# Optimization experiments

Measured on AMD Instinct MI355X. Metric: run time of the kernel, lower is better.

## Reference

```python
import jax, jax.numpy as jnp
import numpy as np
from jax import lax

B, N, K, M, NC = 64, 1024, 20, 256, 40  # clouds, points/cloud, knn k, fps points (ratio 0.25), classes
EPS = 1e-5


def setup_inputs() -> dict:
    key = jax.random.key(0)
    ks = jax.random.split(key, 6)
    w = lambda k, s: jax.random.normal(k, s, jnp.float32) * 0.05
    return {
        "pos": jax.random.normal(ks[0], (B * N, 3), jnp.float32),
        "w1": w(ks[1], (64, 3)), "b1": jnp.zeros(64, jnp.float32),
        "g1": jnp.ones(64, jnp.float32), "be1": jnp.zeros(64, jnp.float32),
        "w2": w(ks[2], (64, 64)), "b2": jnp.zeros(64, jnp.float32),
        "g2": jnp.ones(64, jnp.float32), "be2": jnp.zeros(64, jnp.float32),
        "w_nn1": w(ks[3], (512, 64)), "b_nn1": jnp.zeros(512, jnp.float32),
        "g_bn2": jnp.ones(512, jnp.float32), "be_bn2": jnp.zeros(512, jnp.float32),
        "w_nn4": w(ks[4], (NC, 512)), "b_nn4": jnp.zeros(NC, jnp.float32),
    }


def _knn_idx(p):  # p: [N,3] -> [N,K] neighbor indices, self excluded (loop=False)
    d = jnp.sum(p * p, -1)[:, None] + jnp.sum(p * p, -1)[None, :] - 2.0 * (p @ p.T)
    d = d.at[jnp.arange(N), jnp.arange(N)].set(jnp.inf)
    _, idx = lax.top_k(-d, K)
    return idx


def _fps_idx(p):  # p: [N,3] -> [M] farthest-point-sampling indices (deterministic start at 0)
    def step(carry, _):
        dist, last = carry
        d = jnp.sum((p - p[last]) ** 2, -1)
        dist = jnp.minimum(dist, d)
        nxt = jnp.argmax(dist).astype(jnp.int32)
        return (dist, nxt), nxt
    init = (jnp.full((N,), 1e38, jnp.float32), jnp.int32(0))
    _, idxs = lax.scan(step, init, None, length=M - 1)
    return jnp.concatenate([jnp.zeros((1,), jnp.int32), idxs])


def _bn(x, g, b, axes):  # batch-norm with batch statistics (training mode)
    m = jnp.mean(x, axes, keepdims=True)
    v = jnp.var(x, axes, keepdims=True)
    return (x - m) * lax.rsqrt(v + EPS) * g + b


def reference(pos, w1, b1, g1, be1, w2, b2, g2, be2,
              w_nn1, b_nn1, g_bn2, be_bn2, w_nn4, b_nn4):
    p = pos.reshape(B, N, 3)
    idx = jax.vmap(_knn_idx)(p)                     # [B,N,K]
    nbr = jax.vmap(lambda pb, ib: pb[ib])(p, idx)   # [B,N,K,3]
    rel = nbr - p[:, :, None, :]                    # edge features (relative positions)
    h = jax.nn.relu(jnp.einsum('bnkc,fc->bnkf', rel, w1) + b1)
    h = _bn(h, g1, be1, (0, 1, 2))
    h = jax.nn.relu(jnp.einsum('bnkf,gf->bnkg', h, w2) + b2)
    h = _bn(h, g2, be2, (0, 1, 2))
    feat = jnp.max(h, axis=2)                       # [B,N,64] edge-conv max aggregation
    fidx = jax.vmap(_fps_idx)(p)                    # [B,M]
    f = jnp.take_along_axis(feat, fidx[:, :, None], axis=1)  # [B,M,64]
    y = jnp.einsum('bmf,hf->bmh', f, w_nn1) + b_nn1  # [B,M,512]
    y = jnp.max(y, axis=1)                           # [B,512]
    y = jax.nn.relu(y)
    y = _bn(y, g_bn2, be_bn2, (0,))
    y = y @ w_nn4.T + b_nn4                          # [B,40]
    return jax.nn.log_softmax(y, axis=1)
```

## Files before the change

kernel.cpp:

```cpp
#include <hip/hip_runtime.h>
#include <hip/hip_bf16.h>
#include <cfloat>
#include <math.h>

#define BB 64
#define NN 1024
#define KNN 20
#define MM 256
#define CC 64
#define HH 512
#define NCLS 40
#define EPSF 1e-5f
#define CNT1 (BB*NN*KNN)

#define IDX_OFF    0
#define MAXH2_OFF  (IDX_OFF + BB*NN*KNN)
#define FIDX_OFF   (MAXH2_OFF + BB*NN*CC)
#define Y_OFF      (FIDX_OFF + BB*MM)
#define ACC_OFF    (Y_OFF + BB*HH)
#define W2T_OFF    (ACC_OFF + 256)
#define B2F_OFF    (W2T_OFF + CC*CC)
#define S2_OFF     (B2F_OFF + CC)
#define T2_OFF     (S2_OFF + CC)
#define S3_OFF     (T2_OFF + CC)
#define T3_OFF     (S3_OFF + HH)

typedef __attribute__((ext_vector_type(8)))  short short8;
typedef __attribute__((ext_vector_type(16))) float f32x16;

static __device__ __forceinline__ unsigned short f2bf(float f) {
  unsigned u = __float_as_uint(f);
  unsigned r = (u + 0x7fffu + ((u >> 16) & 1u)) >> 16;
  return (unsigned short)r;
}

__global__ __launch_bounds__(256) void knn_fps_kernel(const float* __restrict__ pos,
                                                      int* __restrict__ idxg,
                                                      int* __restrict__ fidxg) {
  __shared__ float4 pj[NN];
  if (blockIdx.x >= BB) {
    int blk = blockIdx.x - BB;
    int b  = blk >> 5;
    int nb = blk & 31;
    const float* pb = pos + (size_t)b * NN * 3;
    for (int i = threadIdx.x; i < NN; i += 256) {
      float x = pb[i*3+0], y = pb[i*3+1], z = pb[i*3+2];
      pj[i] = make_float4(x, y, z, (x*x + y*y) + z*z);
    }
    __syncthreads();
    int lane = threadIdx.x & 63;
    int wv   = threadIdx.x >> 6;
    unsigned long long lmask_lt = (1ULL << lane) - 1ULL;

    for (int t = 0; t < 8; ++t) {
      int i = nb*32 + wv*8 + t;
      float4 pi = pj[i];
      unsigned u[16];
#pragma unroll
      for (int q = 0; q < 16; ++q) {
        int j = q*64 + lane;
        float4 pw = pj[j];
        float d = pi.w + pw.w - 2.0f*(pi.x*pw.x + pi.y*pw.y + pi.z*pw.z);
        unsigned bits = __float_as_uint(d);
        bits = (bits & 0x80000000u) ? ~bits : (bits | 0x80000000u);
        if (j == i) bits = 0xFFFFFFFFu;
        u[q] = bits;
      }
      unsigned lmin = u[0];
#pragma unroll
      for (int q = 1; q < 16; ++q) lmin = (u[q] < lmin) ? u[q] : lmin;
      unsigned rmin = lmin, rmax = lmin;
#define KNN_DPP_STEP(C) { \
      unsigned t1 = (unsigned)__builtin_amdgcn_update_dpp((int)rmin, (int)rmin, (C), 0xf, 0xf, false); \
      unsigned t2 = (unsigned)__builtin_amdgcn_update_dpp((int)rmax, (int)rmax, (C), 0xf, 0xf, false); \
      rmin = (t1 < rmin) ? t1 : rmin; rmax = (t2 > rmax) ? t2 : rmax; }
      KNN_DPP_STEP(0x111)
      KNN_DPP_STEP(0x112)
      KNN_DPP_STEP(0x114)
      KNN_DPP_STEP(0x118)
      KNN_DPP_STEP(0x142)
      KNN_DPP_STEP(0x143)
#undef KNN_DPP_STEP
      unsigned plo = ((unsigned)__builtin_amdgcn_readlane((int)rmin, 63)) >> 16;
      unsigned phi = ((unsigned)__builtin_amdgcn_readlane((int)rmax, 63)) >> 16;
      int cntHi = -1;
      while (plo < phi) {
        unsigned pmid = (plo + phi) >> 1;
        unsigned tmid = (pmid << 16) | 0xFFFFu;
        int cnt = 0;
#pragma unroll
        for (int q = 0; q < 16; ++q)
          cnt += (int)__popcll(__ballot(u[q] <= tmid));
        if (cnt >= KNN) { phi = pmid; cntHi = cnt; } else plo = pmid + 1;
      }
      unsigned tstar = (phi << 16) | 0xFFFFu;
      unsigned bbase = phi << 16;
      int* op = idxg + (size_t)(b*NN + i) * KNN;
      if (cntHi < 0) {
        cntHi = 0;
#pragma unroll
        for (int q = 0; q < 16; ++q)
          cntHi += (int)__popcll(__ballot(u[q] <= tstar));
      }
      if (cntHi == KNN) {
        int base = 0;
#pragma unroll
        for (int q = 0; q < 16; ++q) {
          bool pred = (u[q] <= tstar);
          unsigned long long mask = __ballot((int)pred);
          if (pred) op[base + (int)__popcll(mask & lmask_lt)] = q*64 + lane;
          base += (int)__popcll(mask);
        }
      } else {
        unsigned lo2 = bbase, hi2 = tstar;
        while (lo2 < hi2) {
          unsigned mid = lo2 + ((hi2 - lo2) >> 1);
          int cnt = 0;
#pragma unroll
          for (int q = 0; q < 16; ++q)
            cnt += (int)__popcll(__ballot(u[q] <= mid));
          if (cnt >= KNN) hi2 = mid; else lo2 = mid + 1;
        }
        unsigned xstar = lo2;
        int base = 0;
#pragma unroll
        for (int q = 0; q < 16; ++q) {
          bool pred = (u[q] < xstar);
          unsigned long long mask = __ballot((int)pred);
          if (pred) op[base + (int)__popcll(mask & lmask_lt)] = q*64 + lane;
          base += (int)__popcll(mask);
        }
        for (int q = 0; q < 16 && base < KNN; ++q) {
          bool pred = (u[q] == xstar);
          unsigned long long mask = __ballot((int)pred);
          if (pred) {
            int pos_ = base + (int)__popcll(mask & lmask_lt);
            if (pos_ < KNN) op[pos_] = q*64 + lane;
          }
          base += (int)__popcll(mask);
        }
      }
    }
  } else {
    int b = blockIdx.x;
    const float* pb = pos + (size_t)b * NN * 3;
    for (int i = threadIdx.x; i < NN; i += 256)
      pj[i] = make_float4(pb[i*3], pb[i*3+1], pb[i*3+2], 0.f);
    __syncthreads();
    if (threadIdx.x >= 64) return;
    int lane = threadIdx.x;
    float px[16], py[16], pz[16], dist[16];
#pragma unroll
    for (int q = 0; q < 16; ++q) {
      float4 p = pj[q*64 + lane];
      px[q] = p.x; py[q] = p.y; pz[q] = p.z;
      dist[q] = 1e38f;
    }
    if (lane == 0) fidxg[b*MM] = 0;
    int cur = 0;
    for (int m = 1; m < MM; ++m) {
      float4 cp = pj[cur];
#pragma unroll
      for (int q = 0; q < 16; ++q) {
        float dx = __fsub_rn(px[q], cp.x);
        float dy = __fsub_rn(py[q], cp.y);
        float dz = __fsub_rn(pz[q], cp.z);
        float dd = __fadd_rn(__fadd_rn(__fmul_rn(dx,dx), __fmul_rn(dy,dy)), __fmul_rn(dz,dz));
        dist[q] = fminf(dist[q], dd);
      }
      float t8[8];
#pragma unroll
      for (int q = 0; q < 8; ++q) t8[q] = fmaxf(dist[q], dist[q + 8]);
#pragma unroll
      for (int q = 0; q < 4; ++q) t8[q] = fmaxf(t8[q], t8[q + 4]);
      float lmax = fmaxf(fmaxf(t8[0], t8[1]), fmaxf(t8[2], t8[3]));
      float r = lmax;
#define FPS_VMAX_STEP(C) { \
      int tt = __builtin_amdgcn_update_dpp(__float_as_int(r), __float_as_int(r), (C), 0xf, 0xf, false); \
      r = fmaxf(r, __int_as_float(tt)); }
      FPS_VMAX_STEP(0x111)
      FPS_VMAX_STEP(0x112)
      FPS_VMAX_STEP(0x114)
      FPS_VMAX_STEP(0x118)
      FPS_VMAX_STEP(0x142)
      FPS_VMAX_STEP(0x143)
#undef FPS_VMAX_STEP
      float wmax = __int_as_float(__builtin_amdgcn_readlane(__float_as_int(r), 63));
      unsigned ci = 0xFFFFFFFFu;
#pragma unroll
      for (int q = 15; q >= 0; --q)
        if (dist[q] == wmax) ci = (unsigned)(q*64 + lane);
#define FPS_IMIN_STEP(C) { \
      unsigned tt = (unsigned)__builtin_amdgcn_update_dpp((int)ci, (int)ci, (C), 0xf, 0xf, false); \
      ci = (tt < ci) ? tt : ci; }
      FPS_IMIN_STEP(0x111)
      FPS_IMIN_STEP(0x112)
      FPS_IMIN_STEP(0x114)
      FPS_IMIN_STEP(0x118)
      FPS_IMIN_STEP(0x142)
      FPS_IMIN_STEP(0x143)
#undef FPS_IMIN_STEP
      cur = (int)(unsigned)__builtin_amdgcn_readlane((int)ci, 63);
      if (lane == 0) fidxg[b*MM + m] = cur;
    }
  }
}

__global__ __launch_bounds__(256) void stats1_kernel(const float* __restrict__ pos,
    const int* __restrict__ idxg, const float* __restrict__ w1,
    const float* __restrict__ b1, float* __restrict__ acc) {
  int b = blockIdx.x >> 4;
  int nb = blockIdx.x & 15;
  __shared__ float px[NN], py[NN], pz[NN];
  __shared__ float relx[4][KNN], rely[4][KNN], relz[4][KNN];
  __shared__ float red[4][CC];
  const float* pb = pos + (size_t)b*NN*3;
  for (int i = threadIdx.x; i < NN; i += 256) {
    px[i] = pb[i*3+0]; py[i] = pb[i*3+1]; pz[i] = pb[i*3+2];
  }
  int c = threadIdx.x & 63, w = threadIdx.x >> 6;
  float w1x = w1[c*3+0], w1y = w1[c*3+1], w1z = w1[c*3+2], b1c = b1[c];
  float s = 0.f, ss = 0.f;
  __syncthreads();
  for (int it = 0; it < 16; ++it) {
    int n0 = nb*64 + it*4;
    if (threadIdx.x < 80) {
      int wv = threadIdx.x / KNN, k = threadIdx.x % KNN;
      int n = n0 + wv;
      int j = idxg[(size_t)(b*NN + n)*KNN + k];
      relx[wv][k] = px[j] - px[n];
      rely[wv][k] = py[j] - py[n];
      relz[wv][k] = pz[j] - pz[n];
    }
    __syncthreads();
#pragma unroll
    for (int k = 0; k < KNN; ++k) {
      float h = fmaxf(relx[w][k]*w1x + rely[w][k]*w1y + relz[w][k]*w1z + b1c, 0.f);
      s += h; ss += h*h;
    }
    __syncthreads();
  }
  red[w][c] = s; __syncthreads();
  if (w == 0) atomicAdd(&acc[c], red[0][c]+red[1][c]+red[2][c]+red[3][c]);
  __syncthreads();
  red[w][c] = ss; __syncthreads();
  if (w == 0) atomicAdd(&acc[64+c], red[0][c]+red[1][c]+red[2][c]+red[3][c]);
}

__global__ void fold1_kernel(const float* __restrict__ acc, const float* __restrict__ g1,
    const float* __restrict__ be1, const float* __restrict__ w2, const float* __restrict__ b2,
    unsigned short* __restrict__ w2bf, float* __restrict__ b2f) {
  __shared__ float s1[CC], t1[CC];
  int tid = threadIdx.x;
  if (tid < CC) {
    float cnt = (float)CNT1;
    float m = acc[tid] / cnt;
    float v = acc[64+tid] / cnt - m*m;
    float sc = g1[tid] * rsqrtf(v + EPSF);
    s1[tid] = sc; t1[tid] = be1[tid] - m*sc;
  }
  __syncthreads();
  int frag = tid >> 6;
  int lane = tid & 63;
  int nt = frag >> 2, ks = frag & 3;
  int cout = nt*32 + (lane & 31);
  int cin0 = ks*16 + (lane >> 5)*8;
  for (int j = 0; j < 8; ++j) {
    int cin = cin0 + j;
    w2bf[((size_t)frag*64 + lane)*8 + j] = f2bf(w2[cout*CC + cin] * s1[cin]);
  }
  if (tid < CC) {
    float accb = b2[tid];
    for (int ci = 0; ci < CC; ++ci) accb += t1[ci]*w2[tid*CC + ci];
    b2f[tid] = accb;
  }
}

__global__ __launch_bounds__(256, 4) void conv2_kernel(const float* __restrict__ pos,
    const int* __restrict__ idxg, const float* __restrict__ w1, const float* __restrict__ b1,
    const unsigned short* __restrict__ w2bf, const float* __restrict__ b2fg,
    float* __restrict__ maxh2, float* __restrict__ acc2) {
  int b = blockIdx.x >> 4;
  int nb = blockIdx.x & 15;
  __shared__ float px[NN], py[NN], pz[NN];
  __shared__ float4 relw[4][KNN];
  __shared__ __align__(16) unsigned short h1s[4][2112];
  __shared__ float redbuf[4][2*CC];
  const float* pb = pos + (size_t)b*NN*3;
  for (int i = threadIdx.x; i < NN; i += 256) {
    px[i] = pb[i*3+0]; py[i] = pb[i*3+1]; pz[i] = pb[i*3+2];
  }
  int lane = threadIdx.x & 63, w = threadIdx.x >> 6;
  int half = lane >> 5, l31 = lane & 31;
  short8 Bf[2][4];
#pragma unroll
  for (int nt = 0; nt < 2; ++nt)
#pragma unroll
    for (int ks = 0; ks < 4; ++ks)
      Bf[nt][ks] = *(const short8*)&w2bf[((size_t)(nt*4+ks)*64 + lane)*8];
  float b2o0 = b2fg[l31], b2o1 = b2fg[32 + l31];
  float w1x = w1[lane*3+0], w1y = w1[lane*3+1], w1z = w1[lane*3+2], b1c = b1[lane];
  unsigned short* hw = h1s[w];
  {
    short8 zz = {0,0,0,0,0,0,0,0};
    for (int z = lane; z < 96; z += 64) {
      int g = z / 12, r = 20 + z % 12;
      *(short8*)&hw[g*264 + r*8] = zz;
    }
  }
  float sA = 0.f, ssA = 0.f, sB = 0.f, ssB = 0.f;
  __syncthreads();
  for (int t = 0; t < 16; ++t) {
    int n = nb*64 + w*16 + t;
    if (lane < KNN) {
      int j = idxg[(size_t)(b*NN + n)*KNN + lane];
      relw[w][lane] = make_float4(px[j]-px[n], py[j]-py[n], pz[j]-pz[n], 0.f);
    }
    int gbase = (lane >> 3)*264 + (lane & 7);
#pragma unroll
    for (int k = 0; k < KNN; ++k) {
      float4 r4 = relw[w][k];
      float h = fmaxf(fmaf(r4.x, w1x, fmaf(r4.y, w1y, fmaf(r4.z, w1z, b1c))), 0.f);
      hw[gbase + k*8] = f2bf(h);
    }
    f32x16 acc0 = {}; f32x16 acc1 = {};
#pragma unroll
    for (int ks = 0; ks < 4; ++ks) {
      short8 A = *(const short8*)&hw[(ks*2 + half)*264 + l31*8];
      acc0 = __builtin_amdgcn_mfma_f32_32x32x16_bf16(A, Bf[0][ks], acc0, 0, 0, 0);
      acc1 = __builtin_amdgcn_mfma_f32_32x32x16_bf16(A, Bf[1][ks], acc1, 0, 0, 0);
    }
    float mx0 = 0.f, mx1 = 0.f;
#pragma unroll
    for (int reg = 0; reg < 8; ++reg) {
      float v0 = fmaxf(acc0[reg] + b2o0, 0.f);
      float v1 = fmaxf(acc1[reg] + b2o1, 0.f);
      sA += v0; ssA += v0*v0; sB += v1; ssB += v1*v1;
      mx0 = fmaxf(mx0, v0); mx1 = fmaxf(mx1, v1);
    }
    if (half == 0) {
#pragma unroll
      for (int reg = 8; reg < 12; ++reg) {
        float v0 = fmaxf(acc0[reg] + b2o0, 0.f);
        float v1 = fmaxf(acc1[reg] + b2o1, 0.f);
        sA += v0; ssA += v0*v0; sB += v1; ssB += v1*v1;
        mx0 = fmaxf(mx0, v0); mx1 = fmaxf(mx1, v1);
      }
    }
    mx0 = fmaxf(mx0, __shfl_xor(mx0, 32, 64));
    mx1 = fmaxf(mx1, __shfl_xor(mx1, 32, 64));
    if (half == 0) {
      float* mp = maxh2 + (size_t)(b*NN + n)*CC;
      mp[l31] = mx0; mp[32 + l31] = mx1;
    }
  }
  sA += __shfl_xor(sA, 32, 64); ssA += __shfl_xor(ssA, 32, 64);
  sB += __shfl_xor(sB, 32, 64); ssB += __shfl_xor(ssB, 32, 64);
  if (half == 0) { redbuf[w][l31] = sA; redbuf[w][32 + l31] = sB; }
  __syncthreads();
  if (w == 0) atomicAdd(&acc2[lane], redbuf[0][lane]+redbuf[1][lane]+redbuf[2][lane]+redbuf[3][lane]);
  __syncthreads();
  if (half == 0) { redbuf[w][l31] = ssA; redbuf[w][32 + l31] = ssB; }
  __syncthreads();
  if (w == 0) atomicAdd(&acc2[64+lane], redbuf[0][lane]+redbuf[1][lane]+redbuf[2][lane]+redbuf[3][lane]);
}

__global__ void fold2_kernel(const float* __restrict__ acc2, const float* __restrict__ g2,
    const float* __restrict__ be2, float* __restrict__ s2, float* __restrict__ t2) {
  int c = threadIdx.x;
  float cnt = (float)CNT1;
  float m = acc2[c]/cnt;
  float v = acc2[64+c]/cnt - m*m;
  float sc = g2[c]*rsqrtf(v+EPSF);
  s2[c] = sc;
  t2[c] = be2[c] - m*sc;
}

__global__ __launch_bounds__(256) void head_kernel(const float* __restrict__ maxh2,
    const int* __restrict__ fidxg, const float* __restrict__ s2g, const float* __restrict__ t2g,
    const float* __restrict__ wnn1, const float* __restrict__ bnn1, float* __restrict__ Y) {
  int b = blockIdx.x >> 2;
  int hc = blockIdx.x & 3;
  __shared__ __align__(16) float ftile[128][CC];
  __shared__ float red2[4][128];
  int hl = threadIdx.x & 63, mseg = threadIdx.x >> 6;
  int hA = hc*128 + hl, hB = hA + 64;
  float4 wva[16], wvb[16];
  const float4* wrA = (const float4*)(wnn1 + (size_t)hA*CC);
  const float4* wrB = (const float4*)(wnn1 + (size_t)hB*CC);
#pragma unroll
  for (int q = 0; q < 16; ++q) { wva[q] = wrA[q]; wvb[q] = wrB[q]; }
  float bestA = -FLT_MAX, bestB = -FLT_MAX;
  const int* fb = fidxg + b*MM;
  for (int chunk = 0; chunk < 2; ++chunk) {
    {
      int row = threadIdx.x & 127, chal = threadIdx.x >> 7;
      int fi = fb[chunk*128 + row];
      const float* src = maxh2 + (size_t)(b*NN + fi)*CC;
      for (int ci = chal*32; ci < chal*32+32; ++ci)
        ftile[row][ci] = s2g[ci]*src[ci] + t2g[ci];
    }
    __syncthreads();
    for (int m = mseg*32; m < mseg*32+32; ++m) {
      float accA = 0.f, accB = 0.f;
#pragma unroll
      for (int cq = 0; cq < 16; ++cq) {
        float4 f = *((const float4*)&ftile[m][cq*4]);
        accA = fmaf(f.x, wva[cq].x, accA);
        accA = fmaf(f.y, wva[cq].y, accA);
        accA = fmaf(f.z, wva[cq].z, accA);
        accA = fmaf(f.w, wva[cq].w, accA);
        accB = fmaf(f.x, wvb[cq].x, accB);
        accB = fmaf(f.y, wvb[cq].y, accB);
        accB = fmaf(f.z, wvb[cq].z, accB);
        accB = fmaf(f.w, wvb[cq].w, accB);
      }
      bestA = fmaxf(bestA, accA);
      bestB = fmaxf(bestB, accB);
    }
    __syncthreads();
  }
  red2[mseg][hl] = bestA;
  red2[mseg][64 + hl] = bestB;
  __syncthreads();
  if (threadIdx.x < 128) {
    int hh = hc*128 + threadIdx.x;
    float v = fmaxf(fmaxf(red2[0][threadIdx.x], red2[1][threadIdx.x]),
                    fmaxf(red2[2][threadIdx.x], red2[3][threadIdx.x])) + bnn1[hh];
    Y[(size_t)b*HH + hh] = fmaxf(v, 0.f);
  }
}

__global__ void bn3_kernel(const float* __restrict__ Y, const float* __restrict__ g,
    const float* __restrict__ be, float* __restrict__ s3, float* __restrict__ t3) {
  int h = blockIdx.x*256 + threadIdx.x;
  float s = 0.f;
  for (int b = 0; b < BB; ++b) s += Y[(size_t)b*HH + h];
  float m = s / (float)BB;
  float v = 0.f;
  for (int b = 0; b < BB; ++b) { float d = Y[(size_t)b*HH + h] - m; v += d*d; }
  v /= (float)BB;
  float sc = g[h] * rsqrtf(v + EPSF);
  s3[h] = sc; t3[h] = be[h] - m*sc;
}

__global__ __launch_bounds__(256) void logits_kernel(const float* __restrict__ Y,
    const float* __restrict__ s3, const float* __restrict__ t3,
    const float* __restrict__ w4, const float* __restrict__ b4, float* __restrict__ out) {
  int b = blockIdx.x;
  __shared__ float ybn[HH];
  __shared__ float lg[NCLS];
  __shared__ float lse;
  for (int hh = threadIdx.x; hh < HH; hh += 256)
    ybn[hh] = Y[(size_t)b*HH + hh]*s3[hh] + t3[hh];
  __syncthreads();
  if (threadIdx.x < NCLS) {
    int j = threadIdx.x;
    float acc = b4[j];
    const float* wr = w4 + (size_t)j*HH;
    for (int ci = 0; ci < HH; ++ci) acc = fmaf(ybn[ci], wr[ci], acc);
    lg[j] = acc;
  }
  __syncthreads();
  if (threadIdx.x == 0) {
    float mx = -FLT_MAX;
    for (int j = 0; j < NCLS; ++j) mx = fmaxf(mx, lg[j]);
    float s = 0.f;
    for (int j = 0; j < NCLS; ++j) s += expf(lg[j] - mx);
    lse = mx + logf(s);
  }
  __syncthreads();
  if (threadIdx.x < NCLS) out[b*NCLS + threadIdx.x] = lg[threadIdx.x] - lse;
}

extern "C" void kernel_launch(void* const* d_in, const int* in_sizes, int n_in,
                              void* d_out, int out_size, void* d_ws, size_t ws_size,
                              hipStream_t stream) {
  const float* pos  = (const float*)d_in[0];
  const float* w1   = (const float*)d_in[1];
  const float* b1   = (const float*)d_in[2];
  const float* g1   = (const float*)d_in[3];
  const float* be1  = (const float*)d_in[4];
  const float* w2   = (const float*)d_in[5];
  const float* b2   = (const float*)d_in[6];
  const float* g2   = (const float*)d_in[7];
  const float* be2  = (const float*)d_in[8];
  const float* wnn1 = (const float*)d_in[9];
  const float* bnn1 = (const float*)d_in[10];
  const float* gbn2 = (const float*)d_in[11];
  const float* bebn2= (const float*)d_in[12];
  const float* wnn4 = (const float*)d_in[13];
  const float* bnn4 = (const float*)d_in[14];
  float* ws = (float*)d_ws;
  int*   idxg  = (int*)(ws + IDX_OFF);
  float* maxh2 = ws + MAXH2_OFF;
  int*   fidxg = (int*)(ws + FIDX_OFF);
  float* Y     = ws + Y_OFF;
  float* acc1  = ws + ACC_OFF;
  float* acc2  = ws + ACC_OFF + 128;
  unsigned short* w2bf = (unsigned short*)(ws + W2T_OFF);
  float* b2f   = ws + B2F_OFF;
  float* s2    = ws + S2_OFF;
  float* t2    = ws + T2_OFF;
  float* s3    = ws + S3_OFF;
  float* t3    = ws + T3_OFF;
  float* outp  = (float*)d_out;

  hipMemsetAsync((void*)(ws + ACC_OFF), 0, 256*sizeof(float), stream);
  knn_fps_kernel<<<BB + BB*32, 256, 0, stream>>>(pos, idxg, fidxg);
  stats1_kernel<<<BB*16, 256, 0, stream>>>(pos, idxg, w1, b1, acc1);
  fold1_kernel<<<1, 512, 0, stream>>>(acc1, g1, be1, w2, b2, w2bf, b2f);
  conv2_kernel<<<BB*16, 256, 0, stream>>>(pos, idxg, w1, b1, w2bf, b2f, maxh2, acc2);
  fold2_kernel<<<1, 64, 0, stream>>>(acc2, g2, be2, s2, t2);
  head_kernel<<<BB*4, 256, 0, stream>>>(maxh2, fidxg, s2, t2, wnn1, bnn1, Y);
  bn3_kernel<<<2, 256, 0, stream>>>(Y, gbn2, bebn2, s3, t3);
  logits_kernel<<<BB, 256, 0, stream>>>(Y, s3, t3, wnn4, bnn4, outp);
}
```

Before: 380.1 us.

## Split serial FPS across three kernels to overlap with KNN and conv stages

The serial farthest-point-sampling loop, which previously ran entirely inside the KNN kernel, is split into three phases (iterations 1-100, 101-150, 151-255). Each phase runs as 64 extra blocks inside the knn, stats1 and conv2 kernels. The running distance array and current index are saved to workspace between phases. The aim is to hide the long single-wave FPS critical path behind the other kernels' work instead of letting it define the knn kernel's tail. The cost is extra state save/restore traffic and extra blocks that compete for CUs in stats1 and conv2.

```diff
diff --git a/kernel.cpp b/kernel.cpp
--- a/kernel.cpp
+++ b/kernel.cpp
@@ -12,6 +12,9 @@
 #define NCLS 40
 #define EPSF 1e-5f
 #define CNT1 (BB*NN*KNN)
+
+#define FPS_R1 101
+#define FPS_R2 151
 
 #define IDX_OFF    0
 #define MAXH2_OFF  (IDX_OFF + BB*NN*KNN)
@@ -24,6 +27,8 @@
 #define T2_OFF     (S2_OFF + CC)
 #define S3_OFF     (T2_OFF + CC)
 #define T3_OFF     (S3_OFF + HH)
+#define FPSD_OFF   (T3_OFF + HH)
+#define FPSC_OFF   (FPSD_OFF + BB*NN)
 
 typedef __attribute__((ext_vector_type(8)))  short short8;
 typedef __attribute__((ext_vector_type(16))) float f32x16;
@@ -34,9 +39,83 @@
   return (unsigned short)r;
 }
 
+static __device__ __forceinline__ void fps_phase(
+    const float* sx, const float* sy, const float* sz,
+    float* fpsd, int* fpsc, int* fidxg, int b, int mStart, int mEnd) {
+  int lane = threadIdx.x;
+  float lx[16], ly[16], lz[16], dist[16];
+#pragma unroll
+  for (int q = 0; q < 16; ++q) {
+    int j = q*64 + lane;
+    lx[q] = sx[j]; ly[q] = sy[j]; lz[q] = sz[j];
+  }
+  int cur;
+  if (mStart <= 1) {
+#pragma unroll
+    for (int q = 0; q < 16; ++q) dist[q] = 1e38f;
+    if (lane == 0) fidxg[b*MM] = 0;
+    cur = 0;
+  } else {
+#pragma unroll
+    for (int q = 0; q < 16; ++q) dist[q] = fpsd[b*NN + q*64 + lane];
+    cur = fpsc[b];
+  }
+  for (int m = mStart; m < mEnd; ++m) {
+    float cpx = sx[cur], cpy = sy[cur], cpz = sz[cur];
+#pragma unroll
+    for (int q = 0; q < 16; ++q) {
+      float dx = __fsub_rn(lx[q], cpx);
+      float dy = __fsub_rn(ly[q], cpy);
+      float dz = __fsub_rn(lz[q], cpz);
+      float dd = __fadd_rn(__fadd_rn(__fmul_rn(dx,dx), __fmul_rn(dy,dy)), __fmul_rn(dz,dz));
+      dist[q] = fminf(dist[q], dd);
+    }
+    float t8[8];
+#pragma unroll
+    for (int q = 0; q < 8; ++q) t8[q] = fmaxf(dist[q], dist[q + 8]);
+#pragma unroll
+    for (int q = 0; q < 4; ++q) t8[q] = fmaxf(t8[q], t8[q + 4]);
+    float r = fmaxf(fmaxf(t8[0], t8[1]), fmaxf(t8[2], t8[3]));
+#define FPS_VMAX_STEP(C) { \
+    int tt = __builtin_amdgcn_update_dpp(__float_as_int(r), __float_as_int(r), (C), 0xf, 0xf, false); \
+    r = fmaxf(r, __int_as_float(tt)); }
+    FPS_VMAX_STEP(0x111)
+    FPS_VMAX_STEP(0x112)
+    FPS_VMAX_STEP(0x114)
+    FPS_VMAX_STEP(0x118)
+    FPS_VMAX_STEP(0x142)
+    FPS_VMAX_STEP(0x143)
+#undef FPS_VMAX_STEP
+    float wmax = __int_as_float(__builtin_amdgcn_readlane(__float_as_int(r), 63));
+    unsigned ci = 0xFFFFFFFFu;
+#pragma unroll
+    for (int q = 15; q >= 0; --q)
+      if (dist[q] == wmax) ci = (unsigned)(q*64 + lane);
+#define FPS_IMIN_STEP(C) { \
+    unsigned tt = (unsigned)__builtin_amdgcn_update_dpp((int)ci, (int)ci, (C), 0xf, 0xf, false); \
+    ci = (tt < ci) ? tt : ci; }
+    FPS_IMIN_STEP(0x111)
+    FPS_IMIN_STEP(0x112)
+    FPS_IMIN_STEP(0x114)
+    FPS_IMIN_STEP(0x118)
+    FPS_IMIN_STEP(0x142)
+    FPS_IMIN_STEP(0x143)
+#undef FPS_IMIN_STEP
+    cur = (int)(unsigned)__builtin_amdgcn_readlane((int)ci, 63);
+    if (lane == 0) fidxg[b*MM + m] = cur;
+  }
+  if (mEnd < MM) {
+#pragma unroll
+    for (int q = 0; q < 16; ++q) fpsd[b*NN + q*64 + lane] = dist[q];
+    if (lane == 0) fpsc[b] = cur;
+  }
+}
+
 __global__ __launch_bounds__(256) void knn_fps_kernel(const float* __restrict__ pos,
                                                       int* __restrict__ idxg,
-                                                      int* __restrict__ fidxg) {
+                                                      int* __restrict__ fidxg,
+                                                      float* __restrict__ fpsd,
+                                                      int* __restrict__ fpsc) {
   __shared__ float4 pj[NN];
   if (blockIdx.x >= BB) {
     int blk = blockIdx.x - BB;
@@ -143,77 +222,39 @@
     }
   } else {
     int b = blockIdx.x;
+    float* base = (float*)pj;
+    float* sx = base; float* sy = base + NN; float* sz = base + 2*NN;
     const float* pb = pos + (size_t)b * NN * 3;
-    for (int i = threadIdx.x; i < NN; i += 256)
-      pj[i] = make_float4(pb[i*3], pb[i*3+1], pb[i*3+2], 0.f);
+    for (int i = threadIdx.x; i < NN; i += 256) {
+      sx[i] = pb[i*3+0]; sy[i] = pb[i*3+1]; sz[i] = pb[i*3+2];
+    }
     __syncthreads();
     if (threadIdx.x >= 64) return;
-    int lane = threadIdx.x;
-    float px[16], py[16], pz[16], dist[16];
-#pragma unroll
-    for (int q = 0; q < 16; ++q) {
-      float4 p = pj[q*64 + lane];
-      px[q] = p.x; py[q] = p.y; pz[q] = p.z;
-      dist[q] = 1e38f;
-    }
-    if (lane == 0) fidxg[b*MM] = 0;
-    int cur = 0;
-    for (int m = 1; m < MM; ++m) {
-      float4 cp = pj[cur];
-#pragma unroll
-      for (int q = 0; q < 16; ++q) {
-        float dx = __fsub_rn(px[q], cp.x);
-        float dy = __fsub_rn(py[q], cp.y);
-        float dz = __fsub_rn(pz[q], cp.z);
-        float dd = __fadd_rn(__fadd_rn(__fmul_rn(dx,dx), __fmul_rn(dy,dy)), __fmul_rn(dz,dz));
-        dist[q] = fminf(dist[q], dd);
-      }
-      float t8[8];
-#pragma unroll
-      for (int q = 0; q < 8; ++q) t8[q] = fmaxf(dist[q], dist[q + 8]);
-#pragma unroll
-      for (int q = 0; q < 4; ++q) t8[q] = fmaxf(t8[q], t8[q + 4]);
-      float lmax = fmaxf(fmaxf(t8[0], t8[1]), fmaxf(t8[2], t8[3]));
-      float r = lmax;
-#define FPS_VMAX_STEP(C) { \
-      int tt = __builtin_amdgcn_update_dpp(__float_as_int(r), __float_as_int(r), (C), 0xf, 0xf, false); \
-      r = fmaxf(r, __int_as_float(tt)); }
-      FPS_VMAX_STEP(0x111)
-      FPS_VMAX_STEP(0x112)
-      FPS_VMAX_STEP(0x114)
-      FPS_VMAX_STEP(0x118)
-      FPS_VMAX_STEP(0x142)
-      FPS_VMAX_STEP(0x143)
-#undef FPS_VMAX_STEP
-      float wmax = __int_as_float(__builtin_amdgcn_readlane(__float_as_int(r), 63));
-      unsigned ci = 0xFFFFFFFFu;
-#pragma unroll
-      for (int q = 15; q >= 0; --q)
-        if (dist[q] == wmax) ci = (unsigned)(q*64 + lane);
-#define FPS_IMIN_STEP(C) { \
-      unsigned tt = (unsigned)__builtin_amdgcn_update_dpp((int)ci, (int)ci, (C), 0xf, 0xf, false); \
-      ci = (tt < ci) ? tt : ci; }
-      FPS_IMIN_STEP(0x111)
-      FPS_IMIN_STEP(0x112)
-      FPS_IMIN_STEP(0x114)
-      FPS_IMIN_STEP(0x118)
-      FPS_IMIN_STEP(0x142)
-      FPS_IMIN_STEP(0x143)
-#undef FPS_IMIN_STEP
-      cur = (int)(unsigned)__builtin_amdgcn_readlane((int)ci, 63);
-      if (lane == 0) fidxg[b*MM + m] = cur;
-    }
+    fps_phase(sx, sy, sz, fpsd, fpsc, fidxg, b, 1, FPS_R1);
   }
 }
 
 __global__ __launch_bounds__(256) void stats1_kernel(const float* __restrict__ pos,
     const int* __restrict__ idxg, const float* __restrict__ w1,
-    const float* __restrict__ b1, float* __restrict__ acc) {
-  int b = blockIdx.x >> 4;
-  int nb = blockIdx.x & 15;
+    const float* __restrict__ b1, float* __restrict__ acc,
+    int* __restrict__ fidxg, float* __restrict__ fpsd, int* __restrict__ fpsc) {
   __shared__ float px[NN], py[NN], pz[NN];
   __shared__ float relx[4][KNN], rely[4][KNN], relz[4][KNN];
   __shared__ float red[4][CC];
+  if (blockIdx.x < BB) {
+    int b = blockIdx.x;
+    const float* pb = pos + (size_t)b*NN*3;
+    for (int i = threadIdx.x; i < NN; i += 256) {
+      px[i] = pb[i*3+0]; py[i] = pb[i*3+1]; pz[i] = pb[i*3+2];
+    }
+    __syncthreads();
+    if (threadIdx.x >= 64) return;
+    fps_phase(px, py, pz, fpsd, fpsc, fidxg, b, FPS_R1, FPS_R2);
+    return;
+  }
+  int blk = blockIdx.x - BB;
+  int b = blk >> 4;
+  int nb = blk & 15;
   const float* pb = pos + (size_t)b*NN*3;
   for (int i = threadIdx.x; i < NN; i += 256) {
     px[i] = pb[i*3+0]; py[i] = pb[i*3+1]; pz[i] = pb[i*3+2];
@@ -279,13 +320,26 @@
 __global__ __launch_bounds__(256, 4) void conv2_kernel(const float* __restrict__ pos,
     const int* __restrict__ idxg, const float* __restrict__ w1, const float* __restrict__ b1,
     const unsigned short* __restrict__ w2bf, const float* __restrict__ b2fg,
-    float* __restrict__ maxh2, float* __restrict__ acc2) {
-  int b = blockIdx.x >> 4;
-  int nb = blockIdx.x & 15;
+    float* __restrict__ maxh2, float* __restrict__ acc2,
+    int* __restrict__ fidxg, float* __restrict__ fpsd, int* __restrict__ fpsc) {
   __shared__ float px[NN], py[NN], pz[NN];
   __shared__ float4 relw[4][KNN];
   __shared__ __align__(16) unsigned short h1s[4][2112];
   __shared__ float redbuf[4][2*CC];
+  if (blockIdx.x < BB) {
+    int b = blockIdx.x;
+    const float* pb = pos + (size_t)b*NN*3;
+    for (int i = threadIdx.x; i < NN; i += 256) {
+      px[i] = pb[i*3+0]; py[i] = pb[i*3+1]; pz[i] = pb[i*3+2];
+    }
+    __syncthreads();
+    if (threadIdx.x >= 64) return;
+    fps_phase(px, py, pz, fpsd, fpsc, fidxg, b, FPS_R2, MM);
+    return;
+  }
+  int blk = blockIdx.x - BB;
+  int b = blk >> 4;
+  int nb = blk & 15;
   const float* pb = pos + (size_t)b*NN*3;
   for (int i = threadIdx.x; i < NN; i += 256) {
     px[i] = pb[i*3+0]; py[i] = pb[i*3+1]; pz[i] = pb[i*3+2];
@@ -504,13 +558,15 @@
   float* t2    = ws + T2_OFF;
   float* s3    = ws + S3_OFF;
   float* t3    = ws + T3_OFF;
+  float* fpsd  = ws + FPSD_OFF;
+  int*   fpsc  = (int*)(ws + FPSC_OFF);
   float* outp  = (float*)d_out;
 
   hipMemsetAsync((void*)(ws + ACC_OFF), 0, 256*sizeof(float), stream);
-  knn_fps_kernel<<<BB + BB*32, 256, 0, stream>>>(pos, idxg, fidxg);
-  stats1_kernel<<<BB*16, 256, 0, stream>>>(pos, idxg, w1, b1, acc1);
+  knn_fps_kernel<<<BB + BB*32, 256, 0, stream>>>(pos, idxg, fidxg, fpsd, fpsc);
+  stats1_kernel<<<BB + BB*16, 256, 0, stream>>>(pos, idxg, w1, b1, acc1, fidxg, fpsd, fpsc);
   fold1_kernel<<<1, 512, 0, stream>>>(acc1, g1, be1, w2, b2, w2bf, b2f);
-  conv2_kernel<<<BB*16, 256, 0, stream>>>(pos, idxg, w1, b1, w2bf, b2f, maxh2, acc2);
+  conv2_kernel<<<BB + BB*16, 256, 0, stream>>>(pos, idxg, w1, b1, w2bf, b2f, maxh2, acc2, fidxg, fpsd, fpsc);
   fold2_kernel<<<1, 64, 0, stream>>>(acc2, g2, be2, s2, t2);
   head_kernel<<<BB*4, 256, 0, stream>>>(maxh2, fidxg, s2, t2, wnn1, bnn1, Y);
   bn3_kernel<<<2, 256, 0, stream>>>(Y, gbn2, bebn2, s3, t3);
```

Measured after the change: 371.4 us. 2.3% less time.
